# Kernel optimization log

Hardware: AMD Instinct MI355X
Metric: run time of the kernel (lower is better)

The kernel has to match this reference:

```python
import jax, jax.numpy as jnp
import numpy as np

B, T, IN_DIM = 8, 1024, 16
D, H, L = 256, 8, 4
DK = D // H
LN_EPS = 1e-5


def setup_inputs() -> dict:
    key = jax.random.key(0)
    ks = jax.random.split(key, 12)
    s = lambda fan_in: 1.0 / np.sqrt(fan_in)
    return {
        "x": jax.random.normal(ks[0], (B, T, IN_DIM), dtype=jnp.float32),
        "Wp": jax.random.normal(ks[1], (IN_DIM, D), dtype=jnp.float32) * s(IN_DIM),
        "bp": jnp.zeros((D,), dtype=jnp.float32),
        "pos": jax.random.normal(ks[2], (1, T, D), dtype=jnp.float32) * 0.1,
        "Wqkv": jax.random.normal(ks[3], (L, D, 3 * D), dtype=jnp.float32) * s(D),
        "bqkv": jnp.zeros((L, 3 * D), dtype=jnp.float32),
        "Wout": jax.random.normal(ks[4], (L, D, D), dtype=jnp.float32) * s(D),
        "bout": jnp.zeros((L, D), dtype=jnp.float32),
        "ln_g": jnp.ones((L, D), dtype=jnp.float32),
        "ln_b": jnp.zeros((L, D), dtype=jnp.float32),
        "Wo": jax.random.normal(ks[5], (D, 3), dtype=jnp.float32) * s(D),
        "bo": jnp.zeros((3,), dtype=jnp.float32),
    }


def _layernorm(x, g, b):
    mu = jnp.mean(x, axis=-1, keepdims=True)
    var = jnp.var(x, axis=-1, keepdims=True)
    return (x - mu) * jax.lax.rsqrt(var + LN_EPS) * g + b


def reference(x, Wp, bp, pos, Wqkv, bqkv, Wout, bout, ln_g, ln_b, Wo, bo):
    # input projection + positional encoding
    h = x @ Wp + bp + pos[:, : x.shape[1], :]  # [B,T,D]
    scale = 1.0 / jnp.sqrt(jnp.float32(DK))
    for l in range(L):
        residual = h
        qkv = h @ Wqkv[l] + bqkv[l]                     # [B,T,3D]
        qkv = qkv.reshape(B, T, 3, H, DK)
        q = qkv[:, :, 0].transpose(0, 2, 1, 3)          # [B,H,T,DK]
        k = qkv[:, :, 1].transpose(0, 2, 1, 3)
        v = qkv[:, :, 2].transpose(0, 2, 1, 3)
        attn = jax.nn.softmax(jnp.einsum("bhqd,bhkd->bhqk", q, k) * scale, axis=-1)
        o = jnp.einsum("bhqk,bhkd->bhqd", attn, v)      # [B,H,T,DK]
        o = o.transpose(0, 2, 1, 3).reshape(B, T, D)
        o = o @ Wout[l] + bout[l]
        h = _layernorm(o + residual, ln_g[l], ln_b[l])
    last = h[:, -1, :]                                   # [B,D]
    return last @ Wo + bo                                # [B,3]
```

## Files before the change

kernel.cpp:

```cpp
#include <hip/hip_runtime.h>
#include <hip/hip_bf16.h>

#define B_ 8
#define T_ 1024
#define IN_DIM_ 16
#define D_ 256
#define H_ 8
#define L_ 4
#define DK_ 32
#define BT_ (B_*T_)
#define LDT 72
#define LDO 264

typedef __attribute__((ext_vector_type(8))) __bf16 bf16x8;
typedef __attribute__((ext_vector_type(8))) unsigned short u16x8;
typedef __attribute__((ext_vector_type(4))) unsigned short u16x4;
typedef __attribute__((ext_vector_type(4))) float f32x4;
typedef __attribute__((ext_vector_type(4))) unsigned int u32x4;

static __device__ __forceinline__ unsigned short f2bf(float f) {
  union { float f; unsigned int u; } c{f};
  unsigned int u = c.u;
  u += 0x7fff + ((u >> 16) & 1);
  return (unsigned short)(u >> 16);
}
static __device__ __forceinline__ float bf2f(unsigned short s) {
  union { unsigned int u; float f; } c{(unsigned int)s << 16};
  return c.f;
}
static __device__ __forceinline__ bf16x8 as_bf(u16x8 v) {
  return __builtin_bit_cast(bf16x8, v);
}

__global__ __launch_bounds__(64) void k_wprep2(
    const float* __restrict__ wqkv, unsigned short* __restrict__ oq,
    const float* __restrict__ wout, unsigned short* __restrict__ oo) {
  int z = blockIdx.z;
  int K = 256;
  int N; const float* inz; unsigned short* outz;
  if (z < 4) {
    N = 768; inz = wqkv + (size_t)z * K * N; outz = oq + (size_t)z * K * N;
  } else {
    N = 256;
    if (blockIdx.x >= 16) return;
    inz = wout + (size_t)(z - 4) * K * N; outz = oo + (size_t)(z - 4) * K * N;
  }
  int nb = blockIdx.x, kb = blockIdx.y;
  int lane = threadIdx.x;
  int li = lane & 15, g = lane >> 4;
  int n = nb * 16 + li;
  int k0 = kb * 32 + g * 8;
  u16x8 v;
  #pragma unroll
  for (int j = 0; j < 8; ++j) v[j] = f2bf(inz[(k0 + j) * N + n]);
  *(u16x8*)(outz + ((nb * (K >> 5) + kb) << 9) + li * 32 + g * 8) = v;
}

__global__ __launch_bounds__(256) void k_proj(
    const float* __restrict__ x, const float* __restrict__ Wp,
    const float* __restrict__ bp, const float* __restrict__ pos,
    unsigned short* __restrict__ hbf) {
  int row = blockIdx.x;
  int c = threadIdx.x;
  int t = row & (T_ - 1);
  float acc = bp[c] + pos[t * D_ + c];
  const float* xr = x + row * IN_DIM_;
  #pragma unroll
  for (int k = 0; k < IN_DIM_; ++k) acc += xr[k] * Wp[k * D_ + c];
  hbf[row * D_ + c] = f2bf(acc);
}

__global__ __launch_bounds__(256) void k_gemm_qkv(
    const unsigned short* __restrict__ A,
    const unsigned short* __restrict__ Btf,
    const float* __restrict__ bias,
    unsigned short* __restrict__ qb, unsigned short* __restrict__ kb,
    unsigned short* __restrict__ vt) {
  __shared__ unsigned short As[128 * LDT];
  int row0 = blockIdx.x * 128;
  int tid = threadIdx.x;
  int lane = tid & 63, w = tid >> 6;
  int g = lane >> 4, li = lane & 15;
  int wr = (w >> 1) * 64, wc = (w & 1) * 32;
  int col0 = blockIdx.y * 64;
  f32x4 acc[4][2] = {};
  for (int k0 = 0; k0 < 256; k0 += 64) {
    __syncthreads();
    int r = tid >> 1, kk = (tid & 1) * 32;
    const unsigned short* src = A + (row0 + r) * 256 + k0 + kk;
    unsigned short* dst = As + r * LDT + kk;
    *(u16x8*)(dst)      = *(const u16x8*)(src);
    *(u16x8*)(dst + 8)  = *(const u16x8*)(src + 8);
    *(u16x8*)(dst + 16) = *(const u16x8*)(src + 16);
    *(u16x8*)(dst + 24) = *(const u16x8*)(src + 24);
    __syncthreads();
    #pragma unroll
    for (int ks = 0; ks < 2; ++ks) {
      int kblk = (k0 >> 5) + ks;
      bf16x8 af[4], bfr[2];
      #pragma unroll
      for (int m = 0; m < 4; ++m)
        af[m] = as_bf(*(const u16x8*)(As + (wr + m * 16 + li) * LDT + ks * 32 + g * 8));
      #pragma unroll
      for (int n = 0; n < 2; ++n) {
        int nblk = (blockIdx.y << 2) + ((w & 1) << 1) + n;
        bfr[n] = as_bf(*(const u16x8*)(Btf + ((nblk * 8 + kblk) << 9) + li * 32 + g * 8));
      }
      #pragma unroll
      for (int m = 0; m < 4; ++m)
        #pragma unroll
        for (int n = 0; n < 2; ++n)
          acc[m][n] = __builtin_amdgcn_mfma_f32_16x16x32_bf16(af[m], bfr[n], acc[m][n], 0, 0, 0);
    }
  }
  const float QSC = 0.25505654f;
  #pragma unroll
  for (int m = 0; m < 4; ++m)
    #pragma unroll
    for (int n = 0; n < 2; ++n) {
      int c = col0 + wc + n * 16 + li;
      int rbase = row0 + wr + m * 16 + g * 4;
      int b = rbase >> 10, t = rbase & (T_ - 1);
      int s = c >> 8, rem = c & 255, hh = rem >> 5, dk = rem & 31;
      if (s == 0) {
        #pragma unroll
        for (int j = 0; j < 4; ++j) {
          float v = (acc[m][n][j] + bias[c]) * QSC;
          qb[(((b * H_ + hh) * T_) + t + j) * DK_ + dk] = f2bf(v);
        }
      } else if (s == 1) {
        #pragma unroll
        for (int j = 0; j < 4; ++j) {
          float v = acc[m][n][j] + bias[c];
          kb[(((b * H_ + hh) * T_) + t + j) * DK_ + dk] = f2bf(v);
        }
      } else {
        u16x4 pk;
        #pragma unroll
        for (int j = 0; j < 4; ++j) pk[j] = f2bf(acc[m][n][j] + bias[c]);
        *(u16x4*)(vt + (b * H_ + hh) * (DK_ * T_) +
                  ((t >> 5) * DK_ + dk) * 32 + (t & 31)) = pk;
      }
    }
}

#define SOFTPV(sA, sB, lrun, bvA, bvB, oac)                                     \
  {                                                                             \
    float p0[4], p1[4];                                                         \
    _Pragma("unroll")                                                           \
    for (int j = 0; j < 4; ++j) {                                               \
      p0[j] = __builtin_amdgcn_exp2f(sA[j]);                                    \
      p1[j] = __builtin_amdgcn_exp2f(sB[j]);                                    \
    }                                                                           \
    lrun += ((p0[0] + p0[1]) + (p0[2] + p0[3])) +                               \
            ((p1[0] + p1[1]) + (p1[2] + p1[3]));                                \
    unsigned int c0, c1, c2, c3;                                                \
    asm("v_cvt_pk_bf16_f32 %0, %1, %2" : "=v"(c0) : "v"(p0[0]), "v"(p0[1]));    \
    asm("v_cvt_pk_bf16_f32 %0, %1, %2" : "=v"(c1) : "v"(p0[2]), "v"(p0[3]));    \
    asm("v_cvt_pk_bf16_f32 %0, %1, %2" : "=v"(c2) : "v"(p1[0]), "v"(p1[1]));    \
    asm("v_cvt_pk_bf16_f32 %0, %1, %2" : "=v"(c3) : "v"(p1[2]), "v"(p1[3]));    \
    asm("v_permlane32_swap_b32 %0, %1" : "+v"(c0), "+v"(c2));                   \
    asm("v_permlane32_swap_b32 %0, %1" : "+v"(c1), "+v"(c3));                   \
    asm("v_permlane16_swap_b32 %0, %1" : "+v"(c0), "+v"(c2));                   \
    asm("v_permlane16_swap_b32 %0, %1" : "+v"(c1), "+v"(c3));                   \
    u32x4 paw; paw[0] = c0; paw[1] = c1; paw[2] = c2; paw[3] = c3;              \
    bf16x8 pa = __builtin_bit_cast(bf16x8, paw);                                \
    __builtin_amdgcn_s_setprio(1);                                              \
    oac[0] = __builtin_amdgcn_mfma_f32_16x16x32_bf16(pa, bvA, oac[0], 0, 0, 0); \
    oac[1] = __builtin_amdgcn_mfma_f32_16x16x32_bf16(pa, bvB, oac[1], 0, 0, 0); \
    __builtin_amdgcn_s_setprio(0);                                              \
  }

__global__ __launch_bounds__(256) void k_attn(
    const unsigned short* __restrict__ qb, const unsigned short* __restrict__ kb,
    const unsigned short* __restrict__ vt, unsigned short* __restrict__ ob) {
  __shared__ float Osh[4][32][33];
  __shared__ float Lsh[4][32];
  int id = blockIdx.x;
  int xcd = id & 7;
  int rest = id >> 3;
  int q0 = (rest & 31) * 32;
  int bh = ((rest >> 5) << 3) | xcd;
  int tid = threadIdx.x, lane = tid & 63, w = tid >> 6;
  int g = lane >> 4, li = lane & 15;
  const unsigned short* Qp = qb + (bh * T_ + q0) * DK_;
  const unsigned short* Kp = kb + bh * T_ * DK_;
  const unsigned short* Vt = vt + bh * DK_ * T_;
  bf16x8 aq0 = as_bf(*(const u16x8*)(Qp + li * DK_ + g * 8));
  bf16x8 aq1 = as_bf(*(const u16x8*)(Qp + (16 + li) * DK_ + g * 8));
  float l_run0 = 0.f, l_run1 = 0.f;
  f32x4 oacc0[2] = {}, oacc1[2] = {};
  for (int kt = w * 256; kt < (w + 1) * 256; kt += 64) {
    const unsigned short* kpA = Kp + kt * DK_;
    bf16x8 bk0 = as_bf(*(const u16x8*)(kpA + li * DK_ + g * 8));
    bf16x8 bk1 = as_bf(*(const u16x8*)(kpA + (16 + li) * DK_ + g * 8));
    bf16x8 bk2 = as_bf(*(const u16x8*)(kpA + (32 + li) * DK_ + g * 8));
    bf16x8 bk3 = as_bf(*(const u16x8*)(kpA + (48 + li) * DK_ + g * 8));
    const unsigned short* vtA = Vt + (kt >> 5) * (DK_ * 32);
    bf16x8 bv0 = as_bf(*(const u16x8*)(vtA + li * 32 + g * 8));
    bf16x8 bv1 = as_bf(*(const u16x8*)(vtA + (16 + li) * 32 + g * 8));
    bf16x8 bv2 = as_bf(*(const u16x8*)(vtA + DK_ * 32 + li * 32 + g * 8));
    bf16x8 bv3 = as_bf(*(const u16x8*)(vtA + DK_ * 32 + (16 + li) * 32 + g * 8));
    {
      f32x4 s0 = {}, s1 = {}, t0 = {}, t1 = {};
      __builtin_amdgcn_s_setprio(1);
      s0 = __builtin_amdgcn_mfma_f32_16x16x32_bf16(bk0, aq0, s0, 0, 0, 0);
      s1 = __builtin_amdgcn_mfma_f32_16x16x32_bf16(bk1, aq0, s1, 0, 0, 0);
      t0 = __builtin_amdgcn_mfma_f32_16x16x32_bf16(bk0, aq1, t0, 0, 0, 0);
      t1 = __builtin_amdgcn_mfma_f32_16x16x32_bf16(bk1, aq1, t1, 0, 0, 0);
      __builtin_amdgcn_s_setprio(0);
      SOFTPV(s0, s1, l_run0, bv0, bv1, oacc0);
      SOFTPV(t0, t1, l_run1, bv0, bv1, oacc1);
    }
    {
      f32x4 s2 = {}, s3 = {}, t2 = {}, t3 = {};
      __builtin_amdgcn_s_setprio(1);
      s2 = __builtin_amdgcn_mfma_f32_16x16x32_bf16(bk2, aq0, s2, 0, 0, 0);
      s3 = __builtin_amdgcn_mfma_f32_16x16x32_bf16(bk3, aq0, s3, 0, 0, 0);
      t2 = __builtin_amdgcn_mfma_f32_16x16x32_bf16(bk2, aq1, t2, 0, 0, 0);
      t3 = __builtin_amdgcn_mfma_f32_16x16x32_bf16(bk3, aq1, t3, 0, 0, 0);
      __builtin_amdgcn_s_setprio(0);
      SOFTPV(s2, s3, l_run0, bv2, bv3, oacc0);
      SOFTPV(t2, t3, l_run1, bv2, bv3, oacc1);
    }
  }
  l_run0 += __shfl_xor(l_run0, 16);
  l_run0 += __shfl_xor(l_run0, 32);
  l_run1 += __shfl_xor(l_run1, 16);
  l_run1 += __shfl_xor(l_run1, 32);
  if (g == 0) { Lsh[w][li] = l_run0; Lsh[w][16 + li] = l_run1; }
  #pragma unroll
  for (int dh = 0; dh < 2; ++dh)
    #pragma unroll
    for (int j = 0; j < 4; ++j) {
      Osh[w][g * 4 + j][dh * 16 + li] = oacc0[dh][j];
      Osh[w][16 + g * 4 + j][dh * 16 + li] = oacc1[dh][j];
    }
  __syncthreads();
  if (tid < 128) {
    int q = tid & 31, dk0 = (tid >> 5) * 8;
    float l = (Lsh[0][q] + Lsh[1][q]) + (Lsh[2][q] + Lsh[3][q]);
    float rl = 1.0f / l;
    int b = bh >> 3, hh = bh & 7;
    u16x8 outv;
    #pragma unroll
    for (int i = 0; i < 8; ++i) {
      float o = (Osh[0][q][dk0 + i] + Osh[1][q][dk0 + i]) +
                (Osh[2][q][dk0 + i] + Osh[3][q][dk0 + i]);
      outv[i] = f2bf(o * rl);
    }
    *(u16x8*)(ob + ((b * T_ + q0 + q) * H_ + hh) * DK_ + dk0) = outv;
  }
}

__global__ __launch_bounds__(256) void k_outln(
    const unsigned short* __restrict__ A,
    const unsigned short* __restrict__ Btf,
    const float* __restrict__ bias,
    const float* __restrict__ gg, const float* __restrict__ bb,
    unsigned short* __restrict__ hbf) {
  __shared__ unsigned short Asp[16 * LDO];
  __shared__ float Ssh[4][16], Qsh[4][16];
  int tid = threadIdx.x, lane = tid & 63, w = tid >> 6;
  int g = lane >> 4, li = lane & 15;
  int row0 = blockIdx.x * 16;
  int c0 = w * 64;
  {
    int r = tid >> 4, kk = (tid & 15) * 16;
    const unsigned short* src = A + (row0 + r) * 256 + kk;
    unsigned short* dst = Asp + r * LDO + kk;
    *(u16x8*)(dst)     = *(const u16x8*)(src);
    *(u16x8*)(dst + 8) = *(const u16x8*)(src + 8);
  }
  __syncthreads();
  f32x4 acc[4] = {};
  for (int k0 = 0; k0 < 256; k0 += 32) {
    int kblk = k0 >> 5;
    bf16x8 af = as_bf(*(const u16x8*)(Asp + li * LDO + k0 + g * 8));
    #pragma unroll
    for (int n = 0; n < 4; ++n) {
      int nblk = w * 4 + n;
      bf16x8 bf = as_bf(*(const u16x8*)(Btf + ((nblk * 8 + kblk) << 9) + li * 32 + g * 8));
      acc[n] = __builtin_amdgcn_mfma_f32_16x16x32_bf16(af, bf, acc[n], 0, 0, 0);
    }
  }
  float uv[4][4];
  float s[4] = {0.f, 0.f, 0.f, 0.f}, q[4] = {0.f, 0.f, 0.f, 0.f};
  #pragma unroll
  for (int n = 0; n < 4; ++n) {
    int c = c0 + n * 16 + li;
    float bs = bias[c];
    #pragma unroll
    for (int j = 0; j < 4; ++j) {
      int r = row0 + g * 4 + j;
      float v = acc[n][j] + bs + bf2f(hbf[r * 256 + c]);
      uv[n][j] = v;
      s[j] += v; q[j] += v * v;
    }
  }
  #pragma unroll
  for (int j = 0; j < 4; ++j) {
    #pragma unroll
    for (int o = 1; o < 16; o <<= 1) {
      s[j] += __shfl_xor(s[j], o);
      q[j] += __shfl_xor(q[j], o);
    }
  }
  if (li == 0) {
    #pragma unroll
    for (int j = 0; j < 4; ++j) {
      Ssh[w][g * 4 + j] = s[j];
      Qsh[w][g * 4 + j] = q[j];
    }
  }
  __syncthreads();
  #pragma unroll
  for (int j = 0; j < 4; ++j) {
    int r = g * 4 + j;
    float st = (Ssh[0][r] + Ssh[1][r]) + (Ssh[2][r] + Ssh[3][r]);
    float qt = (Qsh[0][r] + Qsh[1][r]) + (Qsh[2][r] + Qsh[3][r]);
    float mean = st * (1.0f / D_);
    float var = qt * (1.0f / D_) - mean * mean;
    float rstd = rsqrtf(var + 1e-5f);
    s[j] = mean; q[j] = rstd;
  }
  #pragma unroll
  for (int n = 0; n < 4; ++n) {
    int c = c0 + n * 16 + li;
    float gv = gg[c], bv = bb[c];
    #pragma unroll
    for (int j = 0; j < 4; ++j) {
      int r = row0 + g * 4 + j;
      float y = (uv[n][j] - s[j]) * q[j] * gv + bv;
      hbf[r * 256 + c] = f2bf(y);
    }
  }
}

__global__ void k_final(const unsigned short* __restrict__ hbf,
                        const float* __restrict__ Wo,
                        const float* __restrict__ bo, float* __restrict__ out) {
  int tid = threadIdx.x;
  if (tid >= B_ * 3) return;
  int b = tid / 3, j = tid % 3;
  const unsigned short* hr = hbf + (b * T_ + (T_ - 1)) * D_;
  float acc = bo[j];
  for (int k = 0; k < D_; ++k) acc += bf2f(hr[k]) * Wo[k * 3 + j];
  out[tid] = acc;
}

extern "C" void kernel_launch(void* const* d_in, const int* in_sizes, int n_in,
                              void* d_out, int out_size, void* d_ws, size_t ws_size,
                              hipStream_t stream) {
  const float* x    = (const float*)d_in[0];
  const float* Wp   = (const float*)d_in[1];
  const float* bp   = (const float*)d_in[2];
  const float* pos  = (const float*)d_in[3];
  const float* Wqkv = (const float*)d_in[4];
  const float* bqkv = (const float*)d_in[5];
  const float* Wout = (const float*)d_in[6];
  const float* bout = (const float*)d_in[7];
  const float* ln_g = (const float*)d_in[8];
  const float* ln_b = (const float*)d_in[9];
  const float* Wo   = (const float*)d_in[10];
  const float* bo   = (const float*)d_in[11];

  char* ws = (char*)d_ws;
  unsigned short* hbf = (unsigned short*)(ws);
  unsigned short* qb  = (unsigned short*)(ws + (4u << 20));
  unsigned short* kb  = (unsigned short*)(ws + (8u << 20));
  unsigned short* vt  = (unsigned short*)(ws + (12u << 20));
  unsigned short* ob  = (unsigned short*)(ws + (16u << 20));
  unsigned short* WqkvT = (unsigned short*)(ws + (20u << 20));
  unsigned short* WoutT = (unsigned short*)(ws + (22u << 20));

  k_wprep2<<<dim3(48, 8, 8), 64, 0, stream>>>(Wqkv, WqkvT, Wout, WoutT);
  k_proj<<<BT_, 256, 0, stream>>>(x, Wp, bp, pos, hbf);
  for (int l = 0; l < L_; ++l) {
    k_gemm_qkv<<<dim3(BT_ / 128, 12), 256, 0, stream>>>(
        hbf, WqkvT + l * 768 * 256, bqkv + l * 768, qb, kb, vt);
    k_attn<<<dim3(2048), 256, 0, stream>>>(qb, kb, vt, ob);
    k_outln<<<BT_ / 16, 256, 0, stream>>>(
        ob, WoutT + l * 256 * 256, bout + l * 256,
        ln_g + l * 256, ln_b + l * 256, hbf);
  }
  k_final<<<1, 64, 0, stream>>>(hbf, Wo, bo, (float*)d_out);
}
```

Measured before the change: 185.5 us.

## Store hidden state in MFMA fragment-tiled layout and drop LDS staging in QKV GEMM

The bf16 hidden state is now stored in a 16x32 tiled layout that matches the MFMA operand fragment order. The QKV GEMM therefore loads A fragments straight from global memory and no longer stages them through shared memory with barriers. All producers and consumers of hbf (projection, out-proj/LN residual read and write, final head) switch to the new indexing. This removes LDS traffic and syncs, but it relies on cache reuse for the A tiles and makes the LN kernel's scalar writes more scattered.

```diff
diff --git a/kernel.cpp b/kernel.cpp
--- a/kernel.cpp
+++ b/kernel.cpp
@@ -9,8 +9,9 @@
 #define L_ 4
 #define DK_ 32
 #define BT_ (B_*T_)
-#define LDT 72
 #define LDO 264
+
+#define HT(r, c) ((((r) >> 4) * 8 + ((c) >> 5)) * 512 + (((r) & 15) << 5) + ((c) & 31))
 
 typedef __attribute__((ext_vector_type(8))) __bf16 bf16x8;
 typedef __attribute__((ext_vector_type(8))) unsigned short u16x8;
@@ -67,51 +68,40 @@
   const float* xr = x + row * IN_DIM_;
   #pragma unroll
   for (int k = 0; k < IN_DIM_; ++k) acc += xr[k] * Wp[k * D_ + c];
-  hbf[row * D_ + c] = f2bf(acc);
+  hbf[HT(row, c)] = f2bf(acc);
 }
 
 __global__ __launch_bounds__(256) void k_gemm_qkv(
-    const unsigned short* __restrict__ A,
+    const unsigned short* __restrict__ Af,
     const unsigned short* __restrict__ Btf,
     const float* __restrict__ bias,
     unsigned short* __restrict__ qb, unsigned short* __restrict__ kb,
     unsigned short* __restrict__ vt) {
-  __shared__ unsigned short As[128 * LDT];
-  int row0 = blockIdx.x * 128;
   int tid = threadIdx.x;
   int lane = tid & 63, w = tid >> 6;
   int g = lane >> 4, li = lane & 15;
   int wr = (w >> 1) * 64, wc = (w & 1) * 32;
+  int row0 = blockIdx.x * 128;
   int col0 = blockIdx.y * 64;
+  int rtb = blockIdx.x * 8 + (w >> 1) * 4;
+  int frag = li * 32 + g * 8;
   f32x4 acc[4][2] = {};
-  for (int k0 = 0; k0 < 256; k0 += 64) {
-    __syncthreads();
-    int r = tid >> 1, kk = (tid & 1) * 32;
-    const unsigned short* src = A + (row0 + r) * 256 + k0 + kk;
-    unsigned short* dst = As + r * LDT + kk;
-    *(u16x8*)(dst)      = *(const u16x8*)(src);
-    *(u16x8*)(dst + 8)  = *(const u16x8*)(src + 8);
-    *(u16x8*)(dst + 16) = *(const u16x8*)(src + 16);
-    *(u16x8*)(dst + 24) = *(const u16x8*)(src + 24);
-    __syncthreads();
-    #pragma unroll
-    for (int ks = 0; ks < 2; ++ks) {
-      int kblk = (k0 >> 5) + ks;
-      bf16x8 af[4], bfr[2];
+  #pragma unroll
+  for (int kblk = 0; kblk < 8; ++kblk) {
+    bf16x8 af[4], bfr[2];
+    #pragma unroll
+    for (int m = 0; m < 4; ++m)
+      af[m] = as_bf(*(const u16x8*)(Af + (((rtb + m) * 8 + kblk) << 9) + frag));
+    #pragma unroll
+    for (int n = 0; n < 2; ++n) {
+      int nblk = (blockIdx.y << 2) + ((w & 1) << 1) + n;
+      bfr[n] = as_bf(*(const u16x8*)(Btf + ((nblk * 8 + kblk) << 9) + frag));
+    }
+    #pragma unroll
+    for (int m = 0; m < 4; ++m)
       #pragma unroll
-      for (int m = 0; m < 4; ++m)
-        af[m] = as_bf(*(const u16x8*)(As + (wr + m * 16 + li) * LDT + ks * 32 + g * 8));
-      #pragma unroll
-      for (int n = 0; n < 2; ++n) {
-        int nblk = (blockIdx.y << 2) + ((w & 1) << 1) + n;
-        bfr[n] = as_bf(*(const u16x8*)(Btf + ((nblk * 8 + kblk) << 9) + li * 32 + g * 8));
-      }
-      #pragma unroll
-      for (int m = 0; m < 4; ++m)
-        #pragma unroll
-        for (int n = 0; n < 2; ++n)
-          acc[m][n] = __builtin_amdgcn_mfma_f32_16x16x32_bf16(af[m], bfr[n], acc[m][n], 0, 0, 0);
-    }
+      for (int n = 0; n < 2; ++n)
+        acc[m][n] = __builtin_amdgcn_mfma_f32_16x16x32_bf16(af[m], bfr[n], acc[m][n], 0, 0, 0);
   }
   const float QSC = 0.25505654f;
   #pragma unroll
@@ -293,7 +283,7 @@
     #pragma unroll
     for (int j = 0; j < 4; ++j) {
       int r = row0 + g * 4 + j;
-      float v = acc[n][j] + bs + bf2f(hbf[r * 256 + c]);
+      float v = acc[n][j] + bs + bf2f(hbf[HT(r, c)]);
       uv[n][j] = v;
       s[j] += v; q[j] += v * v;
     }
@@ -332,7 +322,7 @@
     for (int j = 0; j < 4; ++j) {
       int r = row0 + g * 4 + j;
       float y = (uv[n][j] - s[j]) * q[j] * gv + bv;
-      hbf[r * 256 + c] = f2bf(y);
+      hbf[HT(r, c)] = f2bf(y);
     }
   }
 }
@@ -343,9 +333,9 @@
   int tid = threadIdx.x;
   if (tid >= B_ * 3) return;
   int b = tid / 3, j = tid % 3;
-  const unsigned short* hr = hbf + (b * T_ + (T_ - 1)) * D_;
+  int r = b * T_ + (T_ - 1);
   float acc = bo[j];
-  for (int k = 0; k < D_; ++k) acc += bf2f(hr[k]) * Wo[k * 3 + j];
+  for (int k = 0; k < D_; ++k) acc += bf2f(hbf[HT(r, k)]) * Wo[k * 3 + j];
   out[tid] = acc;
 }
 
```

Result: slower. 195.5 us (+5.4%).
